# Kernel optimization log

Hardware: AMD Instinct MI355X
Metric: run time of the kernel (lower is better)

The kernel has to match this reference:

```python
import jax, jax.numpy as jnp
import numpy as np

NEG_INF = -9e15  # matches -9000000000000000.0 in the torch source


def setup_inputs() -> dict:
    key = jax.random.key(0)
    k1, k2, k3, k4 = jax.random.split(key, 4)
    B, H, N, D = 4, 8, 2048, 64
    queries = jax.random.normal(k1, (B, H, N, D), dtype=jnp.float32)
    keys = jax.random.normal(k2, (B, H, N, D), dtype=jnp.float32)
    values = jax.random.normal(k3, (B, H, N, D), dtype=jnp.float32)
    adj = jax.random.randint(k4, (N, N), 0, 2, dtype=jnp.int32)
    return {"queries": queries, "keys": keys, "values": values, "adj": adj}


def reference(queries, keys, values, adj):
    B, H, N, D = queries.shape
    # e = Q K^T / 8  (hard-coded divisor == sqrt(64))
    e = jnp.einsum("bhnd,bhmd->bhnm", queries, keys) / 8.0
    # graph-adjacency mask (adj [N,N] broadcasts over batch and heads)
    att = jnp.where(adj > 0, e, NEG_INF)
    att = jax.nn.softmax(att, axis=-1)
    # dropout p=0.0 / eval mode -> identity
    h_prime = jnp.einsum("bhnm,bhmd->bhnd", att, values)  # [B,H,N,D]
    # original uses .view (flat reshape), NOT a permute
    return h_prime.reshape(N, B, H, D)
```

## Files before the change

kernel.cpp:

```cpp
#include <hip/hip_runtime.h>
#include <math.h>

typedef short short8 __attribute__((ext_vector_type(8)));
typedef float float4_t __attribute__((ext_vector_type(4)));
typedef unsigned uint2_t __attribute__((ext_vector_type(2)));
typedef unsigned short ushort_t;

#define BH   32
#define N_   2048
#define D_   64
#define NCH  32
#define LDP  72
#define KV_ELEMS (BH * N_ * D_)
#define OFF_VF  (KV_ELEMS * 2)
#define OFF_MSK (KV_ELEMS * 4)
#define QSCALE 0.18033688f

__device__ __forceinline__ unsigned pack_bf16(float a, float b) {
  union { float f; unsigned u; } ua{a}, ub{b};
  return __builtin_amdgcn_perm(ub.u + 0x8000u, ua.u + 0x8000u, 0x07060302u);
}

__global__ __launch_bounds__(256) void prep_kernel(
    const float* __restrict__ K, const float* __restrict__ V,
    const int* __restrict__ adj, ushort_t* __restrict__ Kf,
    ushort_t* __restrict__ Vf, unsigned long long* __restrict__ msk) {
  __shared__ __align__(16) float Tc[64 * 68];
  const int blk = blockIdx.x, t = threadIdx.x;

  if (blk < 2048) {
    const bool isK = blk < 1024;
    const int b = isK ? blk : blk - 1024;
    const float* src = (isK ? K : V) + (b >> 5) * (N_ * D_) + (b & 31) * 64 * D_;
#pragma unroll
    for (int i = 0; i < 4; ++i) {
      int idx = i * 256 + t;
      int row = idx >> 4, c4 = (idx & 15) * 4;
      *(float4_t*)&Tc[row * 68 + c4] = *(const float4_t*)(src + row * D_ + c4);
    }
    __syncthreads();
    ushort_t* dst = (isK ? Kf : Vf) + b * 4096;
#pragma unroll
    for (int e = 0; e < 2; ++e) {
      int u = t * 2 + e;
      int g = u >> 6, lane = u & 63;
      int ks = g >> 2, quad = lane >> 4, l16 = lane & 15;
      float v[8];
      if (isK) {
        int nt = g & 3;
        const float* rp = &Tc[(nt * 16 + l16) * 68 + ks * 32 + quad * 8];
        float4_t a = *(const float4_t*)(rp);
        float4_t bq = *(const float4_t*)(rp + 4);
#pragma unroll
        for (int j = 0; j < 4; ++j) { v[j] = a[j]; v[4 + j] = bq[j]; }
      } else {
        int dt = g & 3, d = dt * 16 + l16;
#pragma unroll
        for (int j = 0; j < 8; ++j) {
          int key = 16 * (j & 3) + ks * 8 + quad * 2 + (j >> 2);
          v[j] = Tc[key * 68 + d];
        }
      }
      union { short8 s; unsigned u4[4]; } h;
      h.u4[0] = pack_bf16(v[0], v[1]); h.u4[1] = pack_bf16(v[2], v[3]);
      h.u4[2] = pack_bf16(v[4], v[5]); h.u4[3] = pack_bf16(v[6], v[7]);
      *(short8*)(dst + u * 8) = h.s;
    }
  } else {
    const int row = (blk - 2048) * 4 + (t >> 6);
    const int lane = t & 63;
    unsigned long long keep = 0;
#pragma unroll 8
    for (int i = 0; i < 32; ++i) {
      int a = adj[row * N_ + i * 64 + lane];
      unsigned long long b = __ballot(a > 0);
      if (lane == i) keep = b;
    }
    if (lane < 32) msk[row * 32 + lane] = keep;
  }
}

__global__ __launch_bounds__(256, 4) void attn_main(
    const float* __restrict__ Q, const ushort_t* __restrict__ Kf,
    const ushort_t* __restrict__ Vf, const unsigned long long* __restrict__ msk,
    float* __restrict__ O) {
  __shared__ __align__(16) ushort_t lds_p[4][16 * LDP];

  const int t    = threadIdx.x;
  const int w    = t >> 6;
  const int lane = t & 63;
  const int quad = lane >> 4;
  const int l16  = lane & 15;
  const int bh   = blockIdx.x & (BH - 1);
  const int qt   = blockIdx.x >> 5;
  const int base = bh * (N_ * D_);
  const int qrow0 = qt * 64 + w * 16;

  const ushort_t* Kfb = Kf + (bh * 32) * 4096;
  const ushort_t* Vfb = Vf + (bh * 32) * 4096;
  const unsigned long long* mr = msk + (qrow0 + quad * 4) * 32;

  short8 qf[2];
#pragma unroll
  for (int ks = 0; ks < 2; ++ks) {
    const float* qp = Q + base + (qrow0 + l16) * D_ + ks * 32 + quad * 8;
    float4_t f0 = *(const float4_t*)(qp);
    float4_t f1 = *(const float4_t*)(qp + 4);
    union { short8 s; unsigned u[4]; } h;
    h.u[0] = pack_bf16(f0[0] * QSCALE, f0[1] * QSCALE);
    h.u[1] = pack_bf16(f0[2] * QSCALE, f0[3] * QSCALE);
    h.u[2] = pack_bf16(f1[0] * QSCALE, f1[1] * QSCALE);
    h.u[3] = pack_bf16(f1[2] * QSCALE, f1[3] * QSCALE);
    qf[ks] = h.s;
  }

  short8 ones;
#pragma unroll
  for (int j = 0; j < 8; ++j) ones[j] = (short)0x3F80;

  float4_t oacc[4];
  float4_t osum;
#pragma unroll
  for (int dt = 0; dt < 4; ++dt) oacc[dt] = (float4_t){0.f, 0.f, 0.f, 0.f};
  osum = (float4_t){0.f, 0.f, 0.f, 0.f};

  const int fo = lane * 8;

  for (int c = 0; c < NCH; ++c) {
    const ushort_t* kg = Kfb + c * 4096;
    const ushort_t* vg = Vfb + c * 4096;

    short8 kfr[2][4], vfr[2][4];
#pragma unroll
    for (int ks = 0; ks < 2; ++ks)
#pragma unroll
      for (int nt = 0; nt < 4; ++nt) {
        kfr[ks][nt] = *(const short8*)(kg + (ks * 4 + nt) * 512 + fo);
        vfr[ks][nt] = *(const short8*)(vg + (ks * 4 + nt) * 512 + fo);
      }
    unsigned long long mw[4];
#pragma unroll
    for (int r = 0; r < 4; ++r) mw[r] = mr[r * 32 + c];

    float4_t sacc[4];
#pragma unroll
    for (int nt = 0; nt < 4; ++nt) sacc[nt] = (float4_t){0.f, 0.f, 0.f, 0.f};
#pragma unroll
    for (int ks = 0; ks < 2; ++ks)
#pragma unroll
      for (int nt = 0; nt < 4; ++nt)
        sacc[nt] = __builtin_amdgcn_mfma_f32_16x16x32_bf16(qf[ks], kfr[ks][nt], sacc[nt], 0, 0, 0);

#pragma unroll
    for (int r = 0; r < 4; ++r) {
      unsigned long long sh = mw[r] >> l16;
      unsigned lo = (unsigned)sh, hi = (unsigned)(sh >> 32);
      float p0 = (lo & 1u)       ? exp2f(sacc[0][r]) : 0.f;
      float p1 = (lo & 0x10000u) ? exp2f(sacc[1][r]) : 0.f;
      float p2 = (hi & 1u)       ? exp2f(sacc[2][r]) : 0.f;
      float p3 = (hi & 0x10000u) ? exp2f(sacc[3][r]) : 0.f;
      uint2_t d2;
      d2.x = pack_bf16(p0, p1);
      d2.y = pack_bf16(p2, p3);
      *(uint2_t*)&lds_p[w][(quad * 4 + r) * LDP + (l16 << 2)] = d2;
    }

#pragma unroll
    for (int ks = 0; ks < 2; ++ks) {
      short8 pf = *(const short8*)&lds_p[w][l16 * LDP + ks * 32 + quad * 8];
#pragma unroll
      for (int dt = 0; dt < 4; ++dt)
        oacc[dt] = __builtin_amdgcn_mfma_f32_16x16x32_bf16(pf, vfr[ks][dt], oacc[dt], 0, 0, 0);
      osum = __builtin_amdgcn_mfma_f32_16x16x32_bf16(pf, ones, osum, 0, 0, 0);
    }
  }

#pragma unroll
  for (int r = 0; r < 4; ++r) {
    float inv = 1.f / osum[r];
    int qi = qrow0 + quad * 4 + r;
#pragma unroll
    for (int dt = 0; dt < 4; ++dt)
      O[base + qi * D_ + dt * 16 + l16] = oacc[dt][r] * inv;
  }
}

extern "C" void kernel_launch(void* const* d_in, const int* in_sizes, int n_in,
                              void* d_out, int out_size, void* d_ws, size_t ws_size,
                              hipStream_t stream) {
  const float* Q  = (const float*)d_in[0];
  const float* K  = (const float*)d_in[1];
  const float* V  = (const float*)d_in[2];
  const int* adj  = (const int*)d_in[3];
  float* O        = (float*)d_out;
  ushort_t* Kf    = (ushort_t*)d_ws;
  ushort_t* Vf    = (ushort_t*)((char*)d_ws + OFF_VF);
  unsigned long long* msk = (unsigned long long*)((char*)d_ws + OFF_MSK);

  prep_kernel<<<2560, 256, 0, stream>>>(K, V, adj, Kf, Vf, msk);
  attn_main<<<1024, 256, 0, stream>>>(Q, Kf, Vf, msk, O);
}
```

Measured before the change: 186.3 us.

## Stage K/V chunks through double-buffered LDS with async global-to-LDS loads

```diff
diff --git a/kernel.cpp b/kernel.cpp
--- a/kernel.cpp
+++ b/kernel.cpp
@@ -19,6 +19,12 @@
 __device__ __forceinline__ unsigned pack_bf16(float a, float b) {
   union { float f; unsigned u; } ua{a}, ub{b};
   return __builtin_amdgcn_perm(ub.u + 0x8000u, ua.u + 0x8000u, 0x07060302u);
+}
+
+__device__ __forceinline__ void gload_lds16(const ushort_t* g, ushort_t* l) {
+  __builtin_amdgcn_global_load_lds(
+      (const __attribute__((address_space(1))) unsigned int*)(g),
+      (__attribute__((address_space(3))) unsigned int*)(l), 16, 0, 0);
 }
 
 __global__ __launch_bounds__(256) void prep_kernel(
@@ -80,11 +86,12 @@
   }
 }
 
-__global__ __launch_bounds__(256, 4) void attn_main(
+__global__ __launch_bounds__(512) void attn_main(
     const float* __restrict__ Q, const ushort_t* __restrict__ Kf,
     const ushort_t* __restrict__ Vf, const unsigned long long* __restrict__ msk,
     float* __restrict__ O) {
-  __shared__ __align__(16) ushort_t lds_p[4][16 * LDP];
+  __shared__ __align__(16) ushort_t kv[2][8192];
+  __shared__ __align__(16) ushort_t lds_p[8][16 * LDP];
 
   const int t    = threadIdx.x;
   const int w    = t >> 6;
@@ -94,7 +101,7 @@
   const int bh   = blockIdx.x & (BH - 1);
   const int qt   = blockIdx.x >> 5;
   const int base = bh * (N_ * D_);
-  const int qrow0 = qt * 64 + w * 16;
+  const int qrow0 = qt * 128 + w * 16;
 
   const ushort_t* Kfb = Kf + (bh * 32) * 4096;
   const ushort_t* Vfb = Vf + (bh * 32) * 4096;
@@ -126,30 +133,41 @@
 
   const int fo = lane * 8;
 
+#define STAGE(nb, c)                                                          \
+  do {                                                                        \
+    const ushort_t* _s = (w < 4 ? Kfb + (c)*4096 + w * 1024                   \
+                                : Vfb + (c)*4096 + (w - 4) * 1024) + lane * 8;\
+    ushort_t* _d = &kv[nb][w * 1024];                                         \
+    gload_lds16(_s, _d);                                                      \
+    gload_lds16(_s + 512, _d + 512);                                          \
+  } while (0)
+
+  STAGE(0, 0);
+
+#pragma unroll 2
   for (int c = 0; c < NCH; ++c) {
-    const ushort_t* kg = Kfb + c * 4096;
-    const ushort_t* vg = Vfb + c * 4096;
-
-    short8 kfr[2][4], vfr[2][4];
+    const int cur = c & 1;
+    __syncthreads();
+
+    unsigned long long mw[4];
+#pragma unroll
+    for (int r = 0; r < 4; ++r) mw[r] = mr[r * 32 + c];
+
+    if (c + 1 < NCH) STAGE(cur ^ 1, c + 1);
+
+    const ushort_t* kb = &kv[cur][0];
+    const ushort_t* vb = &kv[cur][4096];
+
+    float4_t sacc[4];
+#pragma unroll
+    for (int nt = 0; nt < 4; ++nt) sacc[nt] = (float4_t){0.f, 0.f, 0.f, 0.f};
 #pragma unroll
     for (int ks = 0; ks < 2; ++ks)
 #pragma unroll
       for (int nt = 0; nt < 4; ++nt) {
-        kfr[ks][nt] = *(const short8*)(kg + (ks * 4 + nt) * 512 + fo);
-        vfr[ks][nt] = *(const short8*)(vg + (ks * 4 + nt) * 512 + fo);
+        short8 kfr = *(const short8*)(kb + (ks * 4 + nt) * 512 + fo);
+        sacc[nt] = __builtin_amdgcn_mfma_f32_16x16x32_bf16(qf[ks], kfr, sacc[nt], 0, 0, 0);
       }
-    unsigned long long mw[4];
-#pragma unroll
-    for (int r = 0; r < 4; ++r) mw[r] = mr[r * 32 + c];
-
-    float4_t sacc[4];
-#pragma unroll
-    for (int nt = 0; nt < 4; ++nt) sacc[nt] = (float4_t){0.f, 0.f, 0.f, 0.f};
-#pragma unroll
-    for (int ks = 0; ks < 2; ++ks)
-#pragma unroll
-      for (int nt = 0; nt < 4; ++nt)
-        sacc[nt] = __builtin_amdgcn_mfma_f32_16x16x32_bf16(qf[ks], kfr[ks][nt], sacc[nt], 0, 0, 0);
 
 #pragma unroll
     for (int r = 0; r < 4; ++r) {
@@ -169,8 +187,10 @@
     for (int ks = 0; ks < 2; ++ks) {
       short8 pf = *(const short8*)&lds_p[w][l16 * LDP + ks * 32 + quad * 8];
 #pragma unroll
-      for (int dt = 0; dt < 4; ++dt)
-        oacc[dt] = __builtin_amdgcn_mfma_f32_16x16x32_bf16(pf, vfr[ks][dt], oacc[dt], 0, 0, 0);
+      for (int dt = 0; dt < 4; ++dt) {
+        short8 vfr = *(const short8*)(vb + (ks * 4 + dt) * 512 + fo);
+        oacc[dt] = __builtin_amdgcn_mfma_f32_16x16x32_bf16(pf, vfr, oacc[dt], 0, 0, 0);
+      }
       osum = __builtin_amdgcn_mfma_f32_16x16x32_bf16(pf, ones, osum, 0, 0, 0);
     }
   }
@@ -198,5 +218,5 @@
   unsigned long long* msk = (unsigned long long*)((char*)d_ws + OFF_MSK);
 
   prep_kernel<<<2560, 256, 0, stream>>>(K, V, adj, Kf, Vf, msk);
-  attn_main<<<1024, 256, 0, stream>>>(Q, Kf, Vf, msk, O);
-}
+  attn_main<<<512, 512, 0, stream>>>(Q, Kf, Vf, msk, O);
+}
```

Measured after the change: 170.8 us. -8.3%, faster.
